# Kernel tuning notes

Measured on AMD Instinct MI355X. Metric: run time of the kernel, lower is better.

The kernel has to match this reference:

```python
import jax, jax.numpy as jnp
import numpy as np

N_NODES = 100000
N_EDGES = 1600000
N_GRAPHS = 2048


def _gcn_conv(x, src, dst, W, b, n_nodes):
    # PyG GCNConv: add self-loops, symmetric norm D^-1/2 A D^-1/2, then linear.
    h = x @ W  # [N, H]
    loop = jnp.arange(n_nodes, dtype=src.dtype)
    s = jnp.concatenate([src, loop])
    d = jnp.concatenate([dst, loop])
    deg = jax.ops.segment_sum(jnp.ones_like(d, dtype=h.dtype), d, num_segments=n_nodes)
    dinv = jax.lax.rsqrt(jnp.maximum(deg, 1.0))
    norm = dinv[s] * dinv[d]  # [E+N]
    msg = h[s] * norm[:, None]  # gathered, normalized messages
    out = jax.ops.segment_sum(msg, d, num_segments=n_nodes)
    return out + b


def _mean_pool(x, batch, n_graphs):
    sums = jax.ops.segment_sum(x, batch, num_segments=n_graphs)
    cnt = jax.ops.segment_sum(jnp.ones((x.shape[0],), x.dtype), batch, num_segments=n_graphs)
    return sums / jnp.maximum(cnt, 1.0)[:, None]


def setup_inputs() -> dict:
    key = jax.random.key(0)
    ks = jax.random.split(key, 8)
    x = jax.random.normal(ks[0], (N_NODES, 128), dtype=jnp.float32)
    edge_index = jax.random.randint(ks[1], (2, N_EDGES), 0, N_NODES, dtype=jnp.int64)
    batch = jnp.sort(jax.random.randint(ks[2], (N_NODES,), 0, N_GRAPHS, dtype=jnp.int64))
    W1 = jax.random.normal(ks[3], (128, 256), dtype=jnp.float32) * 0.05
    b1 = jnp.zeros((256,), jnp.float32)
    W2 = jax.random.normal(ks[4], (256, 256), dtype=jnp.float32) * 0.05
    b2 = jnp.zeros((256,), jnp.float32)
    Wc = jax.random.normal(ks[5], (256, 64), dtype=jnp.float32) * 0.05
    bc = jnp.zeros((64,), jnp.float32)
    return {"x": x, "edge_index": edge_index, "batch": batch,
            "W1": W1, "b1": b1, "W2": W2, "b2": b2, "Wc": Wc, "bc": bc}


def reference(x, edge_index, batch, W1, b1, W2, b2, Wc, bc):
    src, dst = edge_index[0], edge_index[1]
    n = x.shape[0]
    h = jax.nn.relu(_gcn_conv(x, src, dst, W1, b1, n))
    h = jax.nn.relu(_gcn_conv(h, src, dst, W2, b2, n))
    g = _mean_pool(h, batch, N_GRAPHS)  # [G, h2]
    logits = g @ Wc + bc
    return jax.nn.log_softmax(logits, axis=1)
```

## Files before the change

### kernel.cpp

```cpp
#include <hip/hip_runtime.h>
#include <hip/hip_bf16.h>

#define N_NODES 100000
#define N_EDGES 1600000
#define N_GRAPHS 2048
#define F0 128
#define F1 256
#define NCLS 64

#define BSHIFT 9
#define BNODES 512
#define NB 196
#define EPB 4096
#define NCHUNK 391
#define FLATN (NB * NCHUNK)

typedef unsigned int uint32;
typedef unsigned short u16;
typedef u16 u16x8 __attribute__((ext_vector_type(8)));
typedef __bf16 bf16x8 __attribute__((ext_vector_type(8)));
typedef float f32x4 __attribute__((ext_vector_type(4)));

__device__ __forceinline__ float blo(uint32 v) { return __builtin_bit_cast(float, v << 16); }
__device__ __forceinline__ float bhi(uint32 v) { return __builtin_bit_cast(float, v & 0xffff0000u); }
__device__ __forceinline__ float b16f(u16 v) { return __builtin_bit_cast(float, (uint32)v << 16); }
__device__ __forceinline__ u16 f2bf(float f) {
    uint32 u = __builtin_bit_cast(uint32, f);
    u += 0x7fffu + ((u >> 16) & 1u);
    return (u16)(u >> 16);
}
__device__ __forceinline__ uint32 pack2(float a, float b) {
    return (uint32)f2bf(a) | ((uint32)f2bf(b) << 16);
}
__device__ __forceinline__ float ub0(uint32 u) { return (float)(u & 255u); }
__device__ __forceinline__ float ub1(uint32 u) { return (float)((u >> 8) & 255u); }
__device__ __forceinline__ float ub2(uint32 u) { return (float)((u >> 16) & 255u); }
__device__ __forceinline__ float ub3(uint32 u) { return (float)(u >> 24); }

#define SCAN_B 1024

__global__ void scan_partial(const int* __restrict__ in, int n, int* __restrict__ bsum) {
    __shared__ int lds[SCAN_B];
    int i = blockIdx.x * SCAN_B + threadIdx.x;
    lds[threadIdx.x] = (i < n) ? in[i] : 0;
    __syncthreads();
    for (int s = SCAN_B / 2; s > 0; s >>= 1) {
        if (threadIdx.x < s) lds[threadIdx.x] += lds[threadIdx.x + s];
        __syncthreads();
    }
    if (threadIdx.x == 0) bsum[blockIdx.x] = lds[0];
}

__global__ void scan_bsum(int* __restrict__ bsum, int nb) {
    __shared__ int lds[SCAN_B];
    int v = (threadIdx.x < nb) ? bsum[threadIdx.x] : 0;
    lds[threadIdx.x] = v;
    __syncthreads();
    for (int s = 1; s < SCAN_B; s <<= 1) {
        int t = (threadIdx.x >= s) ? lds[threadIdx.x - s] : 0;
        __syncthreads();
        lds[threadIdx.x] += t;
        __syncthreads();
    }
    if (threadIdx.x < nb) bsum[threadIdx.x] = lds[threadIdx.x] - v;
}

__global__ void scan_final(const int* __restrict__ in, int n, const int* __restrict__ bsum,
                           int* __restrict__ out) {
    __shared__ int lds[SCAN_B];
    int i = blockIdx.x * SCAN_B + threadIdx.x;
    int v = (i < n) ? in[i] : 0;
    lds[threadIdx.x] = v;
    __syncthreads();
    for (int s = 1; s < SCAN_B; s <<= 1) {
        int t = (threadIdx.x >= s) ? lds[threadIdx.x - s] : 0;
        __syncthreads();
        lds[threadIdx.x] += t;
        __syncthreads();
    }
    if (i < n) out[i + 1] = lds[threadIdx.x] + bsum[blockIdx.x];
    if (i == 0) out[0] = 0;
}


__global__ __launch_bounds__(256) void hist_pass(const int* __restrict__ dst,
                                                 int* __restrict__ hist) {
    __shared__ int lh[NB];
    int t = threadIdx.x, blk = blockIdx.x;
    if (t < NB) lh[t] = 0;
    __syncthreads();
#pragma unroll
    for (int k = 0; k < EPB / 256; ++k) {
        int e = blk * EPB + k * 256 + t;
        if (e < N_EDGES) atomicAdd(&lh[dst[e] >> BSHIFT], 1);
    }
    __syncthreads();
    if (t < NB) hist[t * NCHUNK + blk] = lh[t];
}

__global__ __launch_bounds__(256) void bin_pairs(const int* __restrict__ src,
                                                 const int* __restrict__ dst,
                                                 const int* __restrict__ histoff,
                                                 uint32* __restrict__ pairs) {
    __shared__ int lbase[NB];
    __shared__ int lcur[NB];
    int t = threadIdx.x, blk = blockIdx.x;
    if (t < NB) {
        lbase[t] = histoff[t * NCHUNK + blk];
        lcur[t] = 0;
    }
    __syncthreads();
#pragma unroll
    for (int k = 0; k < EPB / 256; ++k) {
        int e = blk * EPB + k * 256 + t;
        if (e < N_EDGES) {
            int d = dst[e], s = src[e];
            int b = d >> BSHIFT;
            int r = atomicAdd(&lcur[b], 1);
            pairs[lbase[b] + r] = (uint32)(d & (BNODES - 1)) | ((uint32)s << BSHIFT);
        }
    }
}

__global__ __launch_bounds__(256) void bucket_csr(const uint32* __restrict__ pairs,
                                                  const int* __restrict__ histoff,
                                                  int* __restrict__ offs,
                                                  int* __restrict__ csr,
                                                  float* __restrict__ dinv) {
    __shared__ int lcnt[BNODES];
    __shared__ int lcur[BNODES];
    __shared__ int psum[256];
    int t = threadIdx.x, b = blockIdx.x;
    int n0 = b << BSHIFT;
    int nn = min(BNODES, N_NODES - n0);
    lcnt[t] = 0;
    lcnt[t + 256] = 0;
    __syncthreads();
    int ebase = histoff[b * NCHUNK];
    int eend = (b == NB - 1) ? N_EDGES : histoff[(b + 1) * NCHUNK];
    for (int i = ebase + t; i < eend; i += 256) {
        atomicAdd(&lcnt[pairs[i] & (BNODES - 1)], 1);
    }
    __syncthreads();
    int c0 = lcnt[2 * t], c1 = lcnt[2 * t + 1];
    if (2 * t < nn) dinv[n0 + 2 * t] = rsqrtf((float)(c0 + 1));
    if (2 * t + 1 < nn) dinv[n0 + 2 * t + 1] = rsqrtf((float)(c1 + 1));
    psum[t] = c0 + c1;
    __syncthreads();
    for (int s = 1; s < 256; s <<= 1) {
        int v = (t >= s) ? psum[t - s] : 0;
        __syncthreads();
        psum[t] += v;
        __syncthreads();
    }
    int ep = psum[t] - (c0 + c1);
    lcur[2 * t] = ep;
    lcur[2 * t + 1] = ep + c0;
    if (2 * t < nn) offs[n0 + 2 * t] = ebase + ep;
    if (2 * t + 1 < nn) offs[n0 + 2 * t + 1] = ebase + ep + c0;
    if (b == NB - 1 && t == 0) offs[N_NODES] = N_EDGES;
    __syncthreads();
    for (int i = ebase + t; i < eend; i += 256) {
        uint32 p = pairs[i];
        int r = atomicAdd(&lcur[p & (BNODES - 1)], 1);
        csr[ebase + r] = (int)(p >> BSHIFT);
    }
}


__global__ __launch_bounds__(256) void cast_q8_x(const float* __restrict__ x,
                                                 const float* __restrict__ dinv,
                                                 const int* __restrict__ batch,
                                                 u16* __restrict__ q8,
                                                 float* __restrict__ qs,
                                                 int* __restrict__ gcnt) {
    int node = blockIdx.x * 4 + (threadIdx.x >> 6);
    if (node >= N_NODES) return;
    int lane = threadIdx.x & 63;
    float d = dinv[node];
    float2 v = *(const float2*)&x[(size_t)node * F0 + lane * 2];
    float f0 = v.x * d, f1 = v.y * d;
    float m = fmaxf(fabsf(f0), fabsf(f1));
    for (int s = 32; s > 0; s >>= 1) m = fmaxf(m, __shfl_xor(m, s, 64));
    float inv = (m > 0.f) ? 127.f / m : 0.f;
    int u0 = (int)rintf(f0 * inv) + 128, u1 = (int)rintf(f1 * inv) + 128;
    q8[(size_t)node * 64 + lane] = (u16)((u0 & 255) | ((u1 & 255) << 8));
    if (lane == 0) {
        qs[node] = m * (1.f / 127.f);
        atomicAdd(&gcnt[batch[node]], 1);
    }
}


__global__ void transpose_w2(const float* __restrict__ W1, const float* __restrict__ W2,
                             u16* __restrict__ W1t, u16* __restrict__ W2t) {
    int id = blockIdx.x * blockDim.x + threadIdx.x;
    if (id < F0 * F1) {
        int k = id / F1, n = id % F1;
        W1t[(size_t)n * F0 + k] = f2bf(W1[id]);
    } else {
        int id2 = id - F0 * F1;
        if (id2 < F1 * F1) {
            int k = id2 / F1, n = id2 % F1;
            W2t[(size_t)n * F1 + k] = f2bf(W2[id2]);
        }
    }
}


template <int F>
__global__ __launch_bounds__(256) void aggregate_q8(const void* __restrict__ q8,
                                                    const float* __restrict__ qs,
                                                    const int* __restrict__ offs,
                                                    const int* __restrict__ csr,
                                                    const float* __restrict__ dinv,
                                                    u16* __restrict__ out) {
    constexpr int V = F / 64;
    int node = blockIdx.x * 4 + (threadIdx.x >> 6);
    if (node >= N_NODES) return;
    int lane = threadIdx.x & 63;
    float acc[V];
    float ssum;
    {
        float s = qs[node];
        ssum = s;
        if constexpr (V == 2) {
            uint32 q = (uint32)((const u16*)q8)[(size_t)node * 64 + lane];
            acc[0] = ub0(q) * s;
            acc[1] = ub1(q) * s;
        } else {
            uint32 q = ((const uint32*)q8)[(size_t)node * 64 + lane];
            acc[0] = ub0(q) * s;
            acc[1] = ub1(q) * s;
            acc[2] = ub2(q) * s;
            acc[3] = ub3(q) * s;
        }
    }
    int e0 = offs[node], e1 = offs[node + 1];
    for (int b = e0; b < e1; b += 64) {
        bool valid = (b + lane) < e1;
        int idx = valid ? csr[b + lane] : 0;
        float sv = valid ? qs[idx] : 0.f;
        int cnt = min(64, e1 - b);
        int t = 0;
        for (; t + 4 <= cnt; t += 4) {
            int j0 = __shfl(idx, t), j1 = __shfl(idx, t + 1);
            int j2 = __shfl(idx, t + 2), j3 = __shfl(idx, t + 3);
            float s0 = __shfl(sv, t), s1 = __shfl(sv, t + 1);
            float s2 = __shfl(sv, t + 2), s3 = __shfl(sv, t + 3);
            ssum += (s0 + s1) + (s2 + s3);
            if constexpr (V == 2) {
                uint32 a = (uint32)((const u16*)q8)[(size_t)j0 * 64 + lane];
                uint32 c = (uint32)((const u16*)q8)[(size_t)j1 * 64 + lane];
                uint32 d = (uint32)((const u16*)q8)[(size_t)j2 * 64 + lane];
                uint32 f = (uint32)((const u16*)q8)[(size_t)j3 * 64 + lane];
                acc[0] += ub0(a) * s0 + ub0(c) * s1 + ub0(d) * s2 + ub0(f) * s3;
                acc[1] += ub1(a) * s0 + ub1(c) * s1 + ub1(d) * s2 + ub1(f) * s3;
            } else {
                uint32 a = ((const uint32*)q8)[(size_t)j0 * 64 + lane];
                uint32 c = ((const uint32*)q8)[(size_t)j1 * 64 + lane];
                uint32 d = ((const uint32*)q8)[(size_t)j2 * 64 + lane];
                uint32 f = ((const uint32*)q8)[(size_t)j3 * 64 + lane];
                acc[0] += ub0(a) * s0 + ub0(c) * s1 + ub0(d) * s2 + ub0(f) * s3;
                acc[1] += ub1(a) * s0 + ub1(c) * s1 + ub1(d) * s2 + ub1(f) * s3;
                acc[2] += ub2(a) * s0 + ub2(c) * s1 + ub2(d) * s2 + ub2(f) * s3;
                acc[3] += ub3(a) * s0 + ub3(c) * s1 + ub3(d) * s2 + ub3(f) * s3;
            }
        }
        for (; t < cnt; ++t) {
            int j0 = __shfl(idx, t);
            float s0 = __shfl(sv, t);
            ssum += s0;
            if constexpr (V == 2) {
                uint32 a = (uint32)((const u16*)q8)[(size_t)j0 * 64 + lane];
                acc[0] += ub0(a) * s0;
                acc[1] += ub1(a) * s0;
            } else {
                uint32 a = ((const uint32*)q8)[(size_t)j0 * 64 + lane];
                acc[0] += ub0(a) * s0;
                acc[1] += ub1(a) * s0;
                acc[2] += ub2(a) * s0;
                acc[3] += ub3(a) * s0;
            }
        }
    }
    float di = dinv[node];
    float bias = 128.f * ssum;
    u16* orow = out + (size_t)node * F + lane * V;
    if constexpr (V == 2) {
        *(uint32*)orow = pack2((acc[0] - bias) * di, (acc[1] - bias) * di);
    } else {
        uint2 o;
        o.x = pack2((acc[0] - bias) * di, (acc[1] - bias) * di);
        o.y = pack2((acc[2] - bias) * di, (acc[3] - bias) * di);
        *(uint2*)orow = o;
    }
}


template <int K, bool QUANT>
__global__ __launch_bounds__(256) void gemm_fused(const u16* __restrict__ A,
                                                  const u16* __restrict__ Bt,
                                                  const float* __restrict__ bias,
                                                  const float* __restrict__ dinv,
                                                  int M,
                                                  uint32* __restrict__ q8,
                                                  float* __restrict__ qs,
                                                  const int* __restrict__ batch,
                                                  float* __restrict__ gpool) {
    constexpr int BM = 64, BN = 256, BK = 64, BKP = 72;
    __shared__ __align__(16) char smem[46080];
    u16(*As)[BKP] = (u16(*)[BKP])smem;
    u16(*Bs)[BKP] = (u16(*)[BKP])(smem + BM * BKP * 2);
    int tid = threadIdx.x;
    int row0 = blockIdx.x * BM;
    int lane = tid & 63, wid = tid >> 6;
    int wn = wid * 64;
    int lr = lane & 15, lq = lane >> 4;

    f32x4 acc[4][4];
#pragma unroll
    for (int i = 0; i < 4; ++i)
#pragma unroll
        for (int j = 0; j < 4; ++j) acc[i][j] = (f32x4){0.f, 0.f, 0.f, 0.f};

    for (int k0 = 0; k0 < K; k0 += BK) {
        int c = (tid & 7) * 8;
#pragma unroll
        for (int p = 0; p < 2; ++p) {
            int r = (tid >> 3) + p * 32;
            u16x8 av = {0, 0, 0, 0, 0, 0, 0, 0};
            int gr = row0 + r;
            if (gr < M) av = *(const u16x8*)&A[(size_t)gr * K + k0 + c];
            *(u16x8*)&As[r][c] = av;
        }
#pragma unroll
        for (int p = 0; p < 8; ++p) {
            int r = (tid >> 3) + p * 32;
            *(u16x8*)&Bs[r][c] = *(const u16x8*)&Bt[(size_t)r * K + k0 + c];
        }
        __syncthreads();
#pragma unroll
        for (int kk = 0; kk < BK; kk += 32) {
            bf16x8 af[4], bfr[4];
#pragma unroll
            for (int i = 0; i < 4; ++i)
                af[i] = __builtin_bit_cast(bf16x8, *(const u16x8*)&As[i * 16 + lr][kk + lq * 8]);
#pragma unroll
            for (int j = 0; j < 4; ++j)
                bfr[j] = __builtin_bit_cast(bf16x8, *(const u16x8*)&Bs[wn + j * 16 + lr][kk + lq * 8]);
#pragma unroll
            for (int i = 0; i < 4; ++i)
#pragma unroll
                for (int j = 0; j < 4; ++j)
                    acc[i][j] = __builtin_amdgcn_mfma_f32_16x16x32_bf16(af[i], bfr[j], acc[i][j], 0, 0, 0);
        }
        __syncthreads();
    }

    u16(*P)[260] = (u16(*)[260])smem;
#pragma unroll
    for (int i = 0; i < 4; ++i) {
#pragma unroll
        for (int j = 0; j < 4; ++j) {
            int cl = wn + j * 16 + lr;
            float bv = bias[cl];
#pragma unroll
            for (int r = 0; r < 4; ++r) {
                int rl = i * 16 + lq * 4 + r;
                int row = row0 + rl;
                float v = 0.f;
                if (row < M) {
                    v = fmaxf(acc[i][j][r] + bv, 0.f);
                    if constexpr (QUANT) v *= dinv[row];
                }
                P[rl][cl] = f2bf(v);
            }
        }
    }

    if constexpr (QUANT) {
        float* rmax = (float*)(smem + 33280);
        __syncthreads();
        int row = tid & 63, q = tid >> 6;
        float m = 0.f;
#pragma unroll 8
        for (int i = 0; i < 64; ++i) m = fmaxf(m, b16f(P[row][q * 64 + i]));
        rmax[q * 64 + row] = m;
        __syncthreads();
        m = fmaxf(fmaxf(rmax[row], rmax[64 + row]), fmaxf(rmax[128 + row], rmax[192 + row]));
        int gr = row0 + row;
        if (gr < M) {
            float inv = (m > 0.f) ? 127.f / m : 0.f;
#pragma unroll
            for (int d = 0; d < 16; d += 4) {
                uint32 dw[4];
#pragma unroll
                for (int e = 0; e < 4; ++e) {
                    int cb = q * 64 + (d + e) * 4;
                    uint32 v0 = (uint32)((int)rintf(b16f(P[row][cb + 0]) * inv) + 128);
                    uint32 v1 = (uint32)((int)rintf(b16f(P[row][cb + 1]) * inv) + 128);
                    uint32 v2 = (uint32)((int)rintf(b16f(P[row][cb + 2]) * inv) + 128);
                    uint32 v3 = (uint32)((int)rintf(b16f(P[row][cb + 3]) * inv) + 128);
                    dw[e] = v0 | (v1 << 8) | (v2 << 16) | (v3 << 24);
                }
                *(uint4*)&q8[(size_t)gr * 64 + q * 16 + d] = make_uint4(dw[0], dw[1], dw[2], dw[3]);
            }
            if (q == 0) qs[gr] = m * (1.f / 127.f);
        }
    } else {
        int* batchl = (int*)(smem + 33280);
        if (tid < BM) {
            int row = row0 + tid;
            batchl[tid] = batch[row < M ? row : (M - 1)];
        }
        __syncthreads();
        int c = tid;
        int nrows = min(BM, M - row0);
        int cur = batchl[0];
        float sum = 0.f;
        for (int r = 0; r < nrows; ++r) {
            int gb = batchl[r];
            float v = b16f(P[r][c]);
            if (gb != cur) {
                atomicAdd(&gpool[(size_t)cur * BN + c], sum);
                sum = 0.f;
                cur = gb;
            }
            sum += v;
        }
        atomicAdd(&gpool[(size_t)cur * BN + c], sum);
    }
}


__global__ void classify(const float* __restrict__ gpool, const int* __restrict__ gcnt,
                         const float* __restrict__ Wc, const float* __restrict__ bc,
                         float* __restrict__ out) {
    int gr = blockIdx.x;
    int c = threadIdx.x;
    __shared__ float gl[F1];
    float inv = 1.f / fmaxf((float)gcnt[gr], 1.f);
    for (int k = c; k < F1; k += 64) gl[k] = gpool[(size_t)gr * F1 + k] * inv;
    __syncthreads();
    float acc = bc[c];
    for (int k = 0; k < F1; ++k) acc += gl[k] * Wc[k * NCLS + c];
    float m = acc;
    for (int s = 32; s > 0; s >>= 1) m = fmaxf(m, __shfl_xor(m, s, 64));
    float ex = __expf(acc - m);
    float sum = ex;
    for (int s = 32; s > 0; s >>= 1) sum += __shfl_xor(sum, s, 64);
    out[(size_t)gr * NCLS + c] = acc - m - __logf(sum);
}


extern "C" void kernel_launch(void* const* d_in, const int* in_sizes, int n_in,
                              void* d_out, int out_size, void* d_ws, size_t ws_size,
                              hipStream_t stream) {
    const float* x = (const float*)d_in[0];
    const int* ei = (const int*)d_in[1];
    const int* batch = (const int*)d_in[2];
    const float* W1 = (const float*)d_in[3];
    const float* b1 = (const float*)d_in[4];
    const float* W2 = (const float*)d_in[5];
    const float* b2 = (const float*)d_in[6];
    const float* Wc = (const float*)d_in[7];
    const float* bc = (const float*)d_in[8];
    float* out = (float*)d_out;
    const int* src = ei;
    const int* dst = ei + N_EDGES;

    char* w = (char*)d_ws;
    auto take = [&](size_t n) { char* p = w; w += (n + 255) & ~(size_t)255; return p; };
    float* dinv = (float*)take((size_t)N_NODES * 4);
    int* offs = (int*)take((size_t)(N_NODES + 1) * 4);
    int* hist = (int*)take((size_t)FLATN * 4);
    int* histoff = (int*)take((size_t)(FLATN + 1) * 4);
    int* bsum = (int*)take((size_t)1024 * 4);
    int* gcnt = (int*)take((size_t)N_GRAPHS * 4);
    uint32* pairs = (uint32*)take((size_t)N_EDGES * 4);
    int* csr = (int*)take((size_t)N_EDGES * 4);
    u16* q8x = (u16*)take((size_t)N_NODES * 64 * 2);
    float* qsx = (float*)take((size_t)N_NODES * 4);
    uint32* q8h = (uint32*)take((size_t)N_NODES * 64 * 4);
    float* qsh = (float*)take((size_t)N_NODES * 4);
    u16* aggx = (u16*)take((size_t)N_NODES * F0 * 2);
    u16* agg1 = (u16*)take((size_t)N_NODES * F1 * 2);
    u16* W1t = (u16*)take((size_t)F0 * F1 * 2);
    u16* W2t = (u16*)take((size_t)F1 * F1 * 2);
    float* gpool = (float*)take((size_t)N_GRAPHS * F1 * 4);

    hipMemsetAsync(gcnt, 0, (size_t)N_GRAPHS * 4, stream);
    hipMemsetAsync(gpool, 0, (size_t)N_GRAPHS * F1 * 4, stream);

    hist_pass<<<NCHUNK, 256, 0, stream>>>(dst, hist);
    {
        int nb = (FLATN + SCAN_B - 1) / SCAN_B;
        scan_partial<<<nb, SCAN_B, 0, stream>>>(hist, FLATN, bsum);
        scan_bsum<<<1, SCAN_B, 0, stream>>>(bsum, nb);
        scan_final<<<nb, SCAN_B, 0, stream>>>(hist, FLATN, bsum, histoff);
    }
    bin_pairs<<<NCHUNK, 256, 0, stream>>>(src, dst, histoff, pairs);
    bucket_csr<<<NB, 256, 0, stream>>>(pairs, histoff, offs, csr, dinv);

    transpose_w2<<<(F0 * F1 + F1 * F1 + 255) / 256, 256, 0, stream>>>(W1, W2, W1t, W2t);
    cast_q8_x<<<(N_NODES + 3) / 4, 256, 0, stream>>>(x, dinv, batch, q8x, qsx, gcnt);

    int mblocks = (N_NODES + 63) / 64;

    aggregate_q8<F0><<<(N_NODES + 3) / 4, 256, 0, stream>>>(q8x, qsx, offs, csr, dinv, aggx);
    gemm_fused<F0, true><<<mblocks, 256, 0, stream>>>(aggx, W1t, b1, dinv, N_NODES,
                                                      q8h, qsh, nullptr, nullptr);

    aggregate_q8<F1><<<(N_NODES + 3) / 4, 256, 0, stream>>>(q8h, qsh, offs, csr, dinv, agg1);
    gemm_fused<F1, false><<<mblocks, 256, 0, stream>>>(agg1, W2t, b2, dinv, N_NODES,
                                                       nullptr, nullptr, batch, gpool);

    classify<<<N_GRAPHS, 64, 0, stream>>>(gpool, gcnt, Wc, bc, out);
}
```

Before: 460.4 us.

## Use direct global-to-LDS loads in GEMM, fold scan kernel, cache pairs in LDS

```diff
diff --git a/kernel.cpp b/kernel.cpp
--- a/kernel.cpp
+++ b/kernel.cpp
@@ -37,6 +37,10 @@
 __device__ __forceinline__ float ub2(uint32 u) { return (float)((u >> 16) & 255u); }
 __device__ __forceinline__ float ub3(uint32 u) { return (float)(u >> 24); }
 
+#define GLOAD_LDS16(g, l)                                                                  \
+    __builtin_amdgcn_global_load_lds((const __attribute__((address_space(1))) void*)(g),   \
+                                     (__attribute__((address_space(3))) void*)(l), 16, 0, 0)
+
 #define SCAN_B 1024
 
 __global__ void scan_partial(const int* __restrict__ in, int n, int* __restrict__ bsum) {
@@ -51,23 +55,19 @@
     if (threadIdx.x == 0) bsum[blockIdx.x] = lds[0];
 }
 
-__global__ void scan_bsum(int* __restrict__ bsum, int nb) {
+__global__ void scan_final(const int* __restrict__ in, int n, const int* __restrict__ bsum,
+                           int nb, int* __restrict__ out) {
     __shared__ int lds[SCAN_B];
-    int v = (threadIdx.x < nb) ? bsum[threadIdx.x] : 0;
-    lds[threadIdx.x] = v;
-    __syncthreads();
-    for (int s = 1; s < SCAN_B; s <<= 1) {
-        int t = (threadIdx.x >= s) ? lds[threadIdx.x - s] : 0;
-        __syncthreads();
-        lds[threadIdx.x] += t;
-        __syncthreads();
-    }
-    if (threadIdx.x < nb) bsum[threadIdx.x] = lds[threadIdx.x] - v;
-}
-
-__global__ void scan_final(const int* __restrict__ in, int n, const int* __restrict__ bsum,
-                           int* __restrict__ out) {
-    __shared__ int lds[SCAN_B];
+    __shared__ int bpre[128];
+    if (threadIdx.x < 128) bpre[threadIdx.x] = (threadIdx.x < nb) ? bsum[threadIdx.x] : 0;
+    __syncthreads();
+    for (int s = 1; s < 128; s <<= 1) {
+        int v = (threadIdx.x < 128 && threadIdx.x >= s) ? bpre[threadIdx.x - s] : 0;
+        __syncthreads();
+        if (threadIdx.x < 128) bpre[threadIdx.x] += v;
+        __syncthreads();
+    }
+    int base = (blockIdx.x > 0) ? bpre[blockIdx.x - 1] : 0;
     int i = blockIdx.x * SCAN_B + threadIdx.x;
     int v = (i < n) ? in[i] : 0;
     lds[threadIdx.x] = v;
@@ -78,7 +78,7 @@
         lds[threadIdx.x] += t;
         __syncthreads();
     }
-    if (i < n) out[i + 1] = lds[threadIdx.x] + bsum[blockIdx.x];
+    if (i < n) out[i + 1] = lds[threadIdx.x] + base;
     if (i == 0) out[0] = 0;
 }
 
@@ -122,11 +122,14 @@
     }
 }
 
+#define PCAP 16384
+
 __global__ __launch_bounds__(256) void bucket_csr(const uint32* __restrict__ pairs,
                                                   const int* __restrict__ histoff,
                                                   int* __restrict__ offs,
                                                   int* __restrict__ csr,
                                                   float* __restrict__ dinv) {
+    __shared__ uint32 lp[PCAP];
     __shared__ int lcnt[BNODES];
     __shared__ int lcur[BNODES];
     __shared__ int psum[256];
@@ -139,7 +142,10 @@
     int ebase = histoff[b * NCHUNK];
     int eend = (b == NB - 1) ? N_EDGES : histoff[(b + 1) * NCHUNK];
     for (int i = ebase + t; i < eend; i += 256) {
-        atomicAdd(&lcnt[pairs[i] & (BNODES - 1)], 1);
+        uint32 p = pairs[i];
+        int li = i - ebase;
+        if (li < PCAP) lp[li] = p;
+        atomicAdd(&lcnt[p & (BNODES - 1)], 1);
     }
     __syncthreads();
     int c0 = lcnt[2 * t], c1 = lcnt[2 * t + 1];
@@ -161,7 +167,8 @@
     if (b == NB - 1 && t == 0) offs[N_NODES] = N_EDGES;
     __syncthreads();
     for (int i = ebase + t; i < eend; i += 256) {
-        uint32 p = pairs[i];
+        int li = i - ebase;
+        uint32 p = (li < PCAP) ? lp[li] : pairs[i];
         int r = atomicAdd(&lcur[p & (BNODES - 1)], 1);
         csr[ebase + r] = (int)(p >> BSHIFT);
     }
@@ -308,15 +315,18 @@
                                                   float* __restrict__ qs,
                                                   const int* __restrict__ batch,
                                                   float* __restrict__ gpool) {
-    constexpr int BM = 64, BN = 256, BK = 64, BKP = 72;
-    __shared__ __align__(16) char smem[46080];
-    u16(*As)[BKP] = (u16(*)[BKP])smem;
-    u16(*Bs)[BKP] = (u16(*)[BKP])(smem + BM * BKP * 2);
+    constexpr int BM = 64, BN = 256, BK = 64;
+    __shared__ __align__(16) char smem[40960];
+    u16* As = (u16*)smem;
+    u16* Bs = (u16*)smem + BM * BK;
     int tid = threadIdx.x;
+    int lane = tid & 63;
+    int wid = __builtin_amdgcn_readfirstlane(tid >> 6);
     int row0 = blockIdx.x * BM;
-    int lane = tid & 63, wid = tid >> 6;
+    int lr = lane & 15, lq = lane >> 4;
     int wn = wid * 64;
-    int lr = lane & 15, lq = lane >> 4;
+    int srow = lane >> 3;
+    int schunk = (lane & 7) * 8;
 
     f32x4 acc[4][4];
 #pragma unroll
@@ -325,19 +335,17 @@
         for (int j = 0; j < 4; ++j) acc[i][j] = (f32x4){0.f, 0.f, 0.f, 0.f};
 
     for (int k0 = 0; k0 < K; k0 += BK) {
-        int c = (tid & 7) * 8;
 #pragma unroll
         for (int p = 0; p < 2; ++p) {
-            int r = (tid >> 3) + p * 32;
-            u16x8 av = {0, 0, 0, 0, 0, 0, 0, 0};
-            int gr = row0 + r;
-            if (gr < M) av = *(const u16x8*)&A[(size_t)gr * K + k0 + c];
-            *(u16x8*)&As[r][c] = av;
+            int r0 = wid * 16 + p * 8;
+            const u16* g = A + (size_t)(row0 + r0 + srow) * K + k0 + schunk;
+            GLOAD_LDS16(g, As + r0 * BK);
         }
 #pragma unroll
         for (int p = 0; p < 8; ++p) {
-            int r = (tid >> 3) + p * 32;
-            *(u16x8*)&Bs[r][c] = *(const u16x8*)&Bt[(size_t)r * K + k0 + c];
+            int r0 = wid * 64 + p * 8;
+            const u16* g = Bt + (size_t)(r0 + srow) * K + k0 + schunk;
+            GLOAD_LDS16(g, Bs + r0 * BK);
         }
         __syncthreads();
 #pragma unroll
@@ -345,10 +353,10 @@
             bf16x8 af[4], bfr[4];
 #pragma unroll
             for (int i = 0; i < 4; ++i)
-                af[i] = __builtin_bit_cast(bf16x8, *(const u16x8*)&As[i * 16 + lr][kk + lq * 8]);
+                af[i] = __builtin_bit_cast(bf16x8, *(const u16x8*)&As[(i * 16 + lr) * BK + kk + lq * 8]);
 #pragma unroll
             for (int j = 0; j < 4; ++j)
-                bfr[j] = __builtin_bit_cast(bf16x8, *(const u16x8*)&Bs[wn + j * 16 + lr][kk + lq * 8]);
+                bfr[j] = __builtin_bit_cast(bf16x8, *(const u16x8*)&Bs[(wn + j * 16 + lr) * BK + kk + lq * 8]);
 #pragma unroll
             for (int i = 0; i < 4; ++i)
 #pragma unroll
@@ -484,8 +492,8 @@
     float* qsx = (float*)take((size_t)N_NODES * 4);
     uint32* q8h = (uint32*)take((size_t)N_NODES * 64 * 4);
     float* qsh = (float*)take((size_t)N_NODES * 4);
-    u16* aggx = (u16*)take((size_t)N_NODES * F0 * 2);
-    u16* agg1 = (u16*)take((size_t)N_NODES * F1 * 2);
+    u16* aggx = (u16*)take((size_t)(N_NODES + 64) * F0 * 2);
+    u16* agg1 = (u16*)take((size_t)(N_NODES + 64) * F1 * 2);
     u16* W1t = (u16*)take((size_t)F0 * F1 * 2);
     u16* W2t = (u16*)take((size_t)F1 * F1 * 2);
     float* gpool = (float*)take((size_t)N_GRAPHS * F1 * 4);
@@ -497,8 +505,7 @@
     {
         int nb = (FLATN + SCAN_B - 1) / SCAN_B;
         scan_partial<<<nb, SCAN_B, 0, stream>>>(hist, FLATN, bsum);
-        scan_bsum<<<1, SCAN_B, 0, stream>>>(bsum, nb);
-        scan_final<<<nb, SCAN_B, 0, stream>>>(hist, FLATN, bsum, histoff);
+        scan_final<<<nb, SCAN_B, 0, stream>>>(hist, FLATN, bsum, nb, histoff);
     }
     bin_pairs<<<NCHUNK, 256, 0, stream>>>(src, dst, histoff, pairs);
     bucket_csr<<<NB, 256, 0, stream>>>(pairs, histoff, offs, csr, dinv);
```

Measured after the change: 427.6 us. -7.1%, faster.
